# Kernel optimization log

Hardware: AMD Instinct MI355X
Metric: run time of the kernel (lower is better)

Reference implementation:

```python
import jax, jax.numpy as jnp
import numpy as np

# Offsets from init_kwargs: short- and long-range affinities along x and y.
OFFSETS = ((-1, 0), (0, -1), (-2, 0), (0, -2), (-4, 0), (0, -4), (-8, 0), (0, -8))
B, C, H, W = 1, 1, 4096, 4096
N_LABELS = 64


def setup_inputs() -> dict:
    key = jax.random.key(0)
    # Integer instance labels stored as float (module runs conv on float dtype).
    seg = jax.random.randint(key, (B, C, H, W), 0, N_LABELS).astype(jnp.float32)
    return {"segmentation": seg}


def _shift(x, ox, oy):
    """Zero-padded shift: out[i,j] = x[i+ox, j+oy] (0 outside).

    Exactly reproduces F.conv2d with the 3x3 kernel (-1 at center, +1 at the
    sign-determined corner), dilation=max(1,|off|), padding=max(1,|off|):
    the conv output equals shift(x, ox, oy) - x.
    """
    ax, ay = abs(ox), abs(oy)
    p = jnp.pad(x, ((0, 0), (0, 0), (ax, ax), (ay, ay)))
    Hh, Ww = x.shape[-2], x.shape[-1]
    return p[:, :, ax + ox:ax + ox + Hh, ay + oy:ay + oy + Ww]


def reference(segmentation) -> jnp.ndarray:
    seg = segmentation  # [B,1,H,W]
    affs = []
    for ox, oy in OFFSETS:  # small fixed offset list -> static unroll
        grad = _shift(seg, ox, oy) - seg          # spatial gradient
        aff = jnp.where(grad == 0, jnp.ones_like(grad), jnp.zeros_like(grad))
        affs.append(aff)
    out = jnp.stack(affs, axis=0)  # [O, B, 1, H, W]
    # torch .squeeze(1).squeeze(1) with B=1 -> [O, H, W]
    return out[:, 0, 0]
```

## Files before the change

### kernel.cpp

```cpp
#include <hip/hip_runtime.h>
#include <hip/hip_bf16.h>


#define IMG_H 4096
#define IMG_W 4096

__device__ __forceinline__ float4 eq4(float4 a, float4 b) {
    return make_float4(a.x == b.x ? 1.0f : 0.0f,
                       a.y == b.y ? 1.0f : 0.0f,
                       a.z == b.z ? 1.0f : 0.0f,
                       a.w == b.w ? 1.0f : 0.0f);
}

__global__ __launch_bounds__(256) void GetAffs_83416854823610_kernel(
        const float* __restrict__ seg, float* __restrict__ out) {
    const int i  = blockIdx.y;
    const int j  = (blockIdx.x * blockDim.x + threadIdx.x) * 4;
    const float4 zero4 = make_float4(0.f, 0.f, 0.f, 0.f);

    const size_t rowbase = (size_t)i * IMG_W;
    const float4* rowc = (const float4*)(seg + rowbase);
    const int jq = j >> 2;

    const float4 c = rowc[jq];

    const float4 l1 = (j >= 4) ? rowc[jq - 1] : zero4;
    const float4 l2 = (j >= 8) ? rowc[jq - 2] : zero4;
    float w[12];
    w[0] = l2.x; w[1] = l2.y; w[2]  = l2.z; w[3]  = l2.w;
    w[4] = l1.x; w[5] = l1.y; w[6]  = l1.z; w[7]  = l1.w;
    w[8] = c.x;  w[9] = c.y;  w[10] = c.z;  w[11] = c.w;

    const float4 v1 = (i >= 1) ? *(const float4*)(seg + (size_t)(i - 1) * IMG_W + j) : zero4;
    const float4 v2 = (i >= 2) ? *(const float4*)(seg + (size_t)(i - 2) * IMG_W + j) : zero4;
    const float4 v4 = (i >= 4) ? *(const float4*)(seg + (size_t)(i - 4) * IMG_W + j) : zero4;
    const float4 v8 = (i >= 8) ? *(const float4*)(seg + (size_t)(i - 8) * IMG_W + j) : zero4;

    const float4 h1 = make_float4(w[7], w[8], w[9],  w[10]);
    const float4 h2 = make_float4(w[6], w[7], w[8],  w[9]);
    const float4 h4 = make_float4(w[4], w[5], w[6],  w[7]);
    const float4 h8 = make_float4(w[0], w[1], w[2],  w[3]);

    const size_t HW = (size_t)IMG_H * IMG_W;
    const size_t base = rowbase + (size_t)j;
    *(float4*)(out + 0 * HW + base) = eq4(v1, c);
    *(float4*)(out + 1 * HW + base) = eq4(h1, c);
    *(float4*)(out + 2 * HW + base) = eq4(v2, c);
    *(float4*)(out + 3 * HW + base) = eq4(h2, c);
    *(float4*)(out + 4 * HW + base) = eq4(v4, c);
    *(float4*)(out + 5 * HW + base) = eq4(h4, c);
    *(float4*)(out + 6 * HW + base) = eq4(v8, c);
    *(float4*)(out + 7 * HW + base) = eq4(h8, c);
}

extern "C" void kernel_launch(void* const* d_in, const int* in_sizes, int n_in,
                              void* d_out, int out_size, void* d_ws, size_t ws_size,
                              hipStream_t stream) {
    const float* seg = (const float*)d_in[0];
    float* out = (float*)d_out;
    dim3 grid(IMG_W / (4 * 256), IMG_H);
    dim3 block(256);
    GetAffs_83416854823610_kernel<<<grid, block, 0, stream>>>(seg, out);
}
```

Measured before the change: 624.3 us.

## Process row bands per thread with register ring buffer and nontemporal stores

Each thread now walks a band of 16 rows, keeping the previous 8 rows in a register ring buffer so vertical neighbours are not reloaded from memory. Output writes use nontemporal stores so the large write stream does not pollute the cache. The grid shrinks 16x in the y dimension, which cuts parallelism and adds register pressure from the unrolled band loop. The kernel is dominated by 512MB of writes, so any gain from these changes would come mostly from the store path.

After: 578.0 us. -7.4%, faster.

```diff
diff --git a/kernel.cpp b/kernel.cpp
--- a/kernel.cpp
+++ b/kernel.cpp
@@ -4,6 +4,16 @@
 
 #define IMG_H 4096
 #define IMG_W 4096
+#define BAND  16
+
+typedef float floatx4 __attribute__((ext_vector_type(4)));
+
+__device__ __forceinline__ float4 ld4(const float* p) { return *(const float4*)p; }
+
+__device__ __forceinline__ void st4_nt(float* p, float4 v) {
+    floatx4 x = { v.x, v.y, v.z, v.w };
+    __builtin_nontemporal_store(x, (floatx4*)p);
+}
 
 __device__ __forceinline__ float4 eq4(float4 a, float4 b) {
     return make_float4(a.x == b.x ? 1.0f : 0.0f,
@@ -14,43 +24,50 @@
 
 __global__ __launch_bounds__(256) void GetAffs_83416854823610_kernel(
         const float* __restrict__ seg, float* __restrict__ out) {
-    const int i  = blockIdx.y;
-    const int j  = (blockIdx.x * blockDim.x + threadIdx.x) * 4;
+    const int jq = blockIdx.x * 256 + threadIdx.x;
+    const int j  = jq << 2;
+    const int i0 = blockIdx.y * BAND;
     const float4 zero4 = make_float4(0.f, 0.f, 0.f, 0.f);
 
-    const size_t rowbase = (size_t)i * IMG_W;
-    const float4* rowc = (const float4*)(seg + rowbase);
-    const int jq = j >> 2;
-
-    const float4 c = rowc[jq];
-
-    const float4 l1 = (j >= 4) ? rowc[jq - 1] : zero4;
-    const float4 l2 = (j >= 8) ? rowc[jq - 2] : zero4;
-    float w[12];
-    w[0] = l2.x; w[1] = l2.y; w[2]  = l2.z; w[3]  = l2.w;
-    w[4] = l1.x; w[5] = l1.y; w[6]  = l1.z; w[7]  = l1.w;
-    w[8] = c.x;  w[9] = c.y;  w[10] = c.z;  w[11] = c.w;
-
-    const float4 v1 = (i >= 1) ? *(const float4*)(seg + (size_t)(i - 1) * IMG_W + j) : zero4;
-    const float4 v2 = (i >= 2) ? *(const float4*)(seg + (size_t)(i - 2) * IMG_W + j) : zero4;
-    const float4 v4 = (i >= 4) ? *(const float4*)(seg + (size_t)(i - 4) * IMG_W + j) : zero4;
-    const float4 v8 = (i >= 8) ? *(const float4*)(seg + (size_t)(i - 8) * IMG_W + j) : zero4;
-
-    const float4 h1 = make_float4(w[7], w[8], w[9],  w[10]);
-    const float4 h2 = make_float4(w[6], w[7], w[8],  w[9]);
-    const float4 h4 = make_float4(w[4], w[5], w[6],  w[7]);
-    const float4 h8 = make_float4(w[0], w[1], w[2],  w[3]);
+    float4 hist[8];
+#pragma unroll
+    for (int k = 0; k < 8; ++k) {
+        const int r = i0 - 8 + k;
+        hist[k] = (r >= 0) ? ld4(seg + (size_t)r * IMG_W + j) : zero4;
+    }
 
     const size_t HW = (size_t)IMG_H * IMG_W;
-    const size_t base = rowbase + (size_t)j;
-    *(float4*)(out + 0 * HW + base) = eq4(v1, c);
-    *(float4*)(out + 1 * HW + base) = eq4(h1, c);
-    *(float4*)(out + 2 * HW + base) = eq4(v2, c);
-    *(float4*)(out + 3 * HW + base) = eq4(h2, c);
-    *(float4*)(out + 4 * HW + base) = eq4(v4, c);
-    *(float4*)(out + 5 * HW + base) = eq4(h4, c);
-    *(float4*)(out + 6 * HW + base) = eq4(v8, c);
-    *(float4*)(out + 7 * HW + base) = eq4(h8, c);
+
+#pragma unroll
+    for (int u = 0; u < BAND; ++u) {
+        const int i = i0 + u;
+        const float* row = seg + (size_t)i * IMG_W;
+        const float4 c  = ld4(row + j);
+        const float4 l1 = (j >= 4) ? ld4(row + j - 4) : zero4;
+        const float4 l2 = (j >= 8) ? ld4(row + j - 8) : zero4;
+
+        const float4 v1 = hist[(u + 7) & 7];
+        const float4 v2 = hist[(u + 6) & 7];
+        const float4 v4 = hist[(u + 4) & 7];
+        const float4 v8 = hist[u & 7];
+
+        const float4 h1 = make_float4(l1.w, c.x, c.y, c.z);
+        const float4 h2 = make_float4(l1.z, l1.w, c.x, c.y);
+        const float4 h4 = l1;
+        const float4 h8 = l2;
+
+        const size_t base = (size_t)i * IMG_W + (size_t)j;
+        st4_nt(out + 0 * HW + base, eq4(v1, c));
+        st4_nt(out + 1 * HW + base, eq4(h1, c));
+        st4_nt(out + 2 * HW + base, eq4(v2, c));
+        st4_nt(out + 3 * HW + base, eq4(h2, c));
+        st4_nt(out + 4 * HW + base, eq4(v4, c));
+        st4_nt(out + 5 * HW + base, eq4(h4, c));
+        st4_nt(out + 6 * HW + base, eq4(v8, c));
+        st4_nt(out + 7 * HW + base, eq4(h8, c));
+
+        hist[u & 7] = c;
+    }
 }
 
 extern "C" void kernel_launch(void* const* d_in, const int* in_sizes, int n_in,
@@ -58,7 +75,7 @@
                               hipStream_t stream) {
     const float* seg = (const float*)d_in[0];
     float* out = (float*)d_out;
-    dim3 grid(IMG_W / (4 * 256), IMG_H);
+    dim3 grid((IMG_W / 4) / 256, IMG_H / BAND);
     dim3 block(256);
     GetAffs_83416854823610_kernel<<<grid, block, 0, stream>>>(seg, out);
 }
```
